# Optimization experiments

Hardware: AMD Instinct MI355X
Metric: run time of the kernel (lower is better)

Reference implementation:

```python
import jax, jax.numpy as jnp
import numpy as np

D_MODEL = 2048
N_HEADS = 16
D_HEAD = D_MODEL // N_HEADS  # 128


def setup_inputs() -> dict:
    key = jax.random.key(0)
    ks = jax.random.split(key, 5)
    b, t = 2, 2048
    s = 0.02
    return {
        "x": jax.random.normal(ks[0], (b, t, D_MODEL), dtype=jnp.float32),
        "Wq": jax.random.normal(ks[1], (D_MODEL, D_MODEL), dtype=jnp.float32) * s,
        "Wk": jax.random.normal(ks[2], (D_MODEL, D_HEAD), dtype=jnp.float32) * s,
        "Wv": jax.random.normal(ks[3], (D_MODEL, D_HEAD), dtype=jnp.float32) * s,
        "Wo": jax.random.normal(ks[4], (D_MODEL, D_MODEL), dtype=jnp.float32) * s,
    }


def reference(x, Wq, Wk, Wv, Wo):
    b, t, c = x.shape
    scale = D_HEAD ** -0.5
    # q: [b, h, t, d]; k, v: single shared KV head [b, s, d]
    q = (x @ Wq).reshape(b, t, N_HEADS, D_HEAD).transpose(0, 2, 1, 3)
    k = x @ Wk  # [b, s, d]
    v = x @ Wv  # [b, s, d]
    # broadcast the shared KV head across query heads without materializing copies
    scores = jnp.einsum('bhtd,bsd->bhts', q, k) * scale
    attn = jax.nn.softmax(scores, axis=-1)
    y = jnp.einsum('bhts,bsd->bhtd', attn, v)
    y = y.transpose(0, 2, 1, 3).reshape(b, t, c)
    return y @ Wo
```

## Files before the change

kernel.cpp:

```cpp
#include <hip/hip_runtime.h>

typedef unsigned short ushort_t;
typedef short bf16x8 __attribute__((ext_vector_type(8)));
typedef float f32x4 __attribute__((ext_vector_type(4)));

#define B_    2
#define T_    2048
#define C_    2048
#define H_    16
#define DH_   128
#define BT_   4096
#define NQKV  2304

#define OFF_XB   0UL
#define OFF_WT   16777216UL
#define OFF_WOT  26214400UL
#define OFF_QKV  34603008UL
#define OFF_VT   53477376UL
#define OFF_FLAG 54525952UL

__device__ __forceinline__ ushort_t f2bf(float f) {
  union { float f; unsigned u; } v; v.f = f;
  unsigned r = v.u + 0x7fffu + ((v.u >> 16) & 1u);
  return (ushort_t)(r >> 16);
}
__device__ __forceinline__ float bf2f(ushort_t u) {
  union { float f; unsigned u; } v; v.u = ((unsigned)u) << 16;
  return v.f;
}

__device__ __forceinline__ void gload_lds16(const ushort_t* g, ushort_t* l) {
  __builtin_amdgcn_global_load_lds((__attribute__((address_space(1))) void*)g,
                                   (__attribute__((address_space(3))) void*)l,
                                   16, 0, 0);
}

__global__ void detect_dtype(const ushort_t* x, int* flag) {
  if (threadIdx.x == 0 && blockIdx.x == 0) {
    int sane = 0;
    for (int i = 0; i < 32; ++i) {
      ushort_t u = x[2 * i];
      int e = (u >> 7) & 0xFF;
      if (u == 0 || (e >= 100 && e <= 140)) ++sane;
    }
    *flag = (sane >= 24) ? 1 : 0;
  }
}

__global__ __launch_bounds__(256) void cast_x(const void* __restrict__ xin,
                                              ushort_t* __restrict__ xb,
                                              const int* __restrict__ flag, int n8) {
  int i = blockIdx.x * 256 + threadIdx.x;
  if (i >= n8) return;
  if (*flag) {
    *(bf16x8*)(xb + (size_t)i * 8) = *(const bf16x8*)((const ushort_t*)xin + (size_t)i * 8);
  } else {
    const float* xf = (const float*)xin;
    f32x4 a = *(const f32x4*)(xf + (size_t)i * 8);
    f32x4 b = *(const f32x4*)(xf + (size_t)i * 8 + 4);
    bf16x8 o;
    o[0] = (short)f2bf(a[0]); o[1] = (short)f2bf(a[1]);
    o[2] = (short)f2bf(a[2]); o[3] = (short)f2bf(a[3]);
    o[4] = (short)f2bf(b[0]); o[5] = (short)f2bf(b[1]);
    o[6] = (short)f2bf(b[2]); o[7] = (short)f2bf(b[3]);
    *(bf16x8*)(xb + (size_t)i * 8) = o;
  }
}

__global__ __launch_bounds__(256) void transpose_cast(const void* __restrict__ src,
                                                      ushort_t* __restrict__ dst,
                                                      const int* __restrict__ flag,
                                                      int rows, int cols, int dst_ld,
                                                      int dst_row_off) {
  __shared__ float tile[32][33];
  int c0 = blockIdx.x * 32, r0 = blockIdx.y * 32;
  int tx = threadIdx.x & 31, ty = threadIdx.x >> 5;
  bool isbf = (*flag != 0);
#pragma unroll
  for (int j = 0; j < 4; ++j) {
    int r = r0 + ty + j * 8;
    float v;
    if (isbf) v = bf2f(((const ushort_t*)src)[(size_t)r * cols + c0 + tx]);
    else      v = ((const float*)src)[(size_t)r * cols + c0 + tx];
    tile[ty + j * 8][tx] = v;
  }
  __syncthreads();
#pragma unroll
  for (int j = 0; j < 4; ++j) {
    int c = c0 + ty + j * 8;
    dst[(size_t)(dst_row_off + c) * dst_ld + r0 + tx] = f2bf(tile[tx][ty + j * 8]);
  }
}

__global__ __launch_bounds__(256) void transpose_v(const ushort_t* __restrict__ qkv,
                                                   ushort_t* __restrict__ vT) {
  __shared__ ushort_t tile[32][33];
  int b = blockIdx.z;
  int t0 = blockIdx.x * 32, d0 = blockIdx.y * 32;
  int tx = threadIdx.x & 31, ty = threadIdx.x >> 5;
#pragma unroll
  for (int j = 0; j < 4; ++j) {
    int t = t0 + ty + j * 8;
    tile[ty + j * 8][tx] = qkv[(size_t)(b * T_ + t) * NQKV + 2176 + d0 + tx];
  }
  __syncthreads();
#pragma unroll
  for (int j = 0; j < 4; ++j) {
    int d = d0 + ty + j * 8;
    vT[(size_t)b * (DH_ * T_) + (size_t)d * T_ + t0 + tx] = tile[tx][ty + j * 8];
  }
}

__global__ __launch_bounds__(256) void gemm_bt(const ushort_t* __restrict__ A,
                                               const ushort_t* __restrict__ Bt,
                                               void* __restrict__ Cv,
                                               int M, int N, int K,
                                               int is_final, const int* __restrict__ flag) {
  __shared__ __align__(16) ushort_t As[128 * 32];
  __shared__ __align__(16) ushort_t Bs[128 * 32];
  const int tid = threadIdx.x;
  const int lane = tid & 63;
  const int wid = tid >> 6;
  const int m0 = blockIdx.y * 128;
  const int n0 = blockIdx.x * 128;
  const int wr = wid >> 1, wc = wid & 1;
  const int l15 = lane & 15, l4 = lane >> 4;

  f32x4 zero = {0.f, 0.f, 0.f, 0.f};
  f32x4 acc[4][4];
#pragma unroll
  for (int r = 0; r < 4; ++r)
#pragma unroll
    for (int c = 0; c < 4; ++c) acc[r][c] = zero;

  const ushort_t* ga = A + (size_t)(m0 + (tid >> 2)) * K + (tid & 3) * 8;
  const ushort_t* gb = Bt + (size_t)(n0 + (tid >> 2)) * K + (tid & 3) * 8;
  ushort_t* lA = As + wid * 512;
  ushort_t* lB = Bs + wid * 512;
  const size_t stride64 = (size_t)64 * K;

  for (int k0 = 0; k0 < K; k0 += 32) {
    __syncthreads();
    gload_lds16(ga + k0, lA);
    gload_lds16(ga + k0 + stride64, lA + 2048);
    gload_lds16(gb + k0, lB);
    gload_lds16(gb + k0 + stride64, lB + 2048);
    __syncthreads();

    bf16x8 af[4], bfr[4];
#pragma unroll
    for (int r = 0; r < 4; ++r)
      af[r] = *(const bf16x8*)&As[(wr * 64 + r * 16 + l15) * 32 + l4 * 8];
#pragma unroll
    for (int c = 0; c < 4; ++c)
      bfr[c] = *(const bf16x8*)&Bs[(wc * 64 + c * 16 + l15) * 32 + l4 * 8];
#pragma unroll
    for (int r = 0; r < 4; ++r)
#pragma unroll
      for (int c = 0; c < 4; ++c)
        acc[r][c] = __builtin_amdgcn_mfma_f32_16x16x32_bf16(af[r], bfr[c], acc[r][c], 0, 0, 0);
  }

  const bool f32out = is_final && (*flag == 0);
#pragma unroll
  for (int r = 0; r < 4; ++r) {
#pragma unroll
    for (int c = 0; c < 4; ++c) {
      int row = m0 + wr * 64 + r * 16 + l4 * 4;
      int col = n0 + wc * 64 + c * 16 + l15;
#pragma unroll
      for (int g = 0; g < 4; ++g) {
        if (f32out) ((float*)Cv)[(size_t)(row + g) * N + col] = acc[r][c][g];
        else ((ushort_t*)Cv)[(size_t)(row + g) * N + col] = f2bf(acc[r][c][g]);
      }
    }
  }
}

__global__ __launch_bounds__(512, 4) void attn_kernel(const ushort_t* __restrict__ qkv,
                                                      const ushort_t* __restrict__ vT,
                                                      ushort_t* __restrict__ y) {
  __shared__ __align__(16) ushort_t Ks[64 * 128];
  __shared__ __align__(16) ushort_t Vs[128 * 64];
  __shared__ __align__(16) ushort_t Pl[8][16][72];

  const int tid = threadIdx.x;
  const int lane = tid & 63;
  const int wid = tid >> 6;
  const int h = blockIdx.y * 2 + (wid >> 2);
  const int b = blockIdx.z;
  const int tb = b * T_;
  const int q0 = blockIdx.x * 64 + (wid & 3) * 16;
  const int l15 = lane & 15, l4 = lane >> 4;

  bf16x8 qf[4];
  {
    const ushort_t* qbase = qkv + (size_t)(tb + q0 + l15) * NQKV + h * DH_ + l4 * 8;
#pragma unroll
    for (int ks = 0; ks < 4; ++ks) qf[ks] = *(const bf16x8*)(qbase + ks * 32);
  }

  const ushort_t* ksrc[2];
  const ushort_t* vsrc[2];
  ushort_t* kdst[2];
  ushort_t* vdst[2];
#pragma unroll
  for (int it = 0; it < 2; ++it) {
    int id = tid + it * 512;
    int krow = id >> 4, kslot = id & 15;
    ksrc[it] = qkv + (size_t)(tb + krow) * NQKV + 2048 + ((kslot ^ (krow & 7)) << 3);
    kdst[it] = Ks + (size_t)(it * 512 + (wid << 6)) * 8;
    int vrow = id >> 3, vslot = id & 7;
    vsrc[it] = vT + (size_t)b * (DH_ * T_) + (size_t)vrow * T_ + ((vslot ^ (vrow & 7)) << 3);
    vdst[it] = Vs + (size_t)(it * 512 + (wid << 6)) * 8;
  }

  f32x4 zero = {0.f, 0.f, 0.f, 0.f};
  f32x4 o[8];
#pragma unroll
  for (int i = 0; i < 8; ++i) o[i] = zero;
  float mrow[4] = {-1e30f, -1e30f, -1e30f, -1e30f};
  float lrow[4] = {0.f, 0.f, 0.f, 0.f};
  const float sc = 0.08838834764831845f;

  for (int st = 0; st < 32; ++st) {
    const int s0 = st * 64;
    __syncthreads();
    gload_lds16(ksrc[0] + (size_t)s0 * NQKV, kdst[0]);
    gload_lds16(ksrc[1] + (size_t)s0 * NQKV, kdst[1]);
    gload_lds16(vsrc[0] + s0, vdst[0]);
    gload_lds16(vsrc[1] + s0, vdst[1]);
    __syncthreads();

    f32x4 sa[4];
#pragma unroll
    for (int c = 0; c < 4; ++c) {
      sa[c] = zero;
      int srow = c * 16 + l15;
      int sw = srow & 7;
#pragma unroll
      for (int ks = 0; ks < 4; ++ks) {
        bf16x8 kf = *(const bf16x8*)&Ks[srow * 128 + (((ks * 4 + l4) ^ sw) << 3)];
        sa[c] = __builtin_amdgcn_mfma_f32_16x16x32_bf16(qf[ks], kf, sa[c], 0, 0, 0);
      }
    }

    float alpha[4];
#pragma unroll
    for (int r = 0; r < 4; ++r) {
#pragma unroll
      for (int c = 0; c < 4; ++c) sa[c][r] *= sc;
      float m = fmaxf(fmaxf(sa[0][r], sa[1][r]), fmaxf(sa[2][r], sa[3][r]));
      m = fmaxf(m, __shfl_xor(m, 1));
      m = fmaxf(m, __shfl_xor(m, 2));
      m = fmaxf(m, __shfl_xor(m, 4));
      m = fmaxf(m, __shfl_xor(m, 8));
      float mn = fmaxf(mrow[r], m);
      alpha[r] = __expf(mrow[r] - mn);
      mrow[r] = mn;
      float s = 0.f;
#pragma unroll
      for (int c = 0; c < 4; ++c) {
        float p = __expf(sa[c][r] - mn);
        sa[c][r] = p;
        s += p;
      }
      s += __shfl_xor(s, 1);
      s += __shfl_xor(s, 2);
      s += __shfl_xor(s, 4);
      s += __shfl_xor(s, 8);
      lrow[r] = lrow[r] * alpha[r] + s;
    }

#pragma unroll
    for (int c = 0; c < 4; ++c)
#pragma unroll
      for (int r = 0; r < 4; ++r)
        Pl[wid][l4 * 4 + r][c * 16 + l15] = f2bf(sa[c][r]);

#pragma unroll
    for (int nb = 0; nb < 8; ++nb)
#pragma unroll
      for (int r = 0; r < 4; ++r) o[nb][r] *= alpha[r];

    bf16x8 pa0 = *(const bf16x8*)&Pl[wid][l15][l4 * 8];
    bf16x8 pa1 = *(const bf16x8*)&Pl[wid][l15][32 + l4 * 8];
#pragma unroll
    for (int nb = 0; nb < 8; ++nb) {
      int vrow = nb * 16 + l15;
      int sw = vrow & 7;
      bf16x8 vb0 = *(const bf16x8*)&Vs[vrow * 64 + ((l4 ^ sw) << 3)];
      o[nb] = __builtin_amdgcn_mfma_f32_16x16x32_bf16(pa0, vb0, o[nb], 0, 0, 0);
      bf16x8 vb1 = *(const bf16x8*)&Vs[vrow * 64 + (((4 + l4) ^ sw) << 3)];
      o[nb] = __builtin_amdgcn_mfma_f32_16x16x32_bf16(pa1, vb1, o[nb], 0, 0, 0);
    }
  }

#pragma unroll
  for (int nb = 0; nb < 8; ++nb) {
#pragma unroll
    for (int r = 0; r < 4; ++r) {
      int qrow = tb + q0 + l4 * 4 + r;
      y[(size_t)qrow * C_ + h * DH_ + nb * 16 + l15] = f2bf(o[nb][r] / lrow[r]);
    }
  }
}

extern "C" void kernel_launch(void* const* d_in, const int* in_sizes, int n_in,
                              void* d_out, int out_size, void* d_ws, size_t ws_size,
                              hipStream_t stream) {
  (void)in_sizes; (void)n_in; (void)out_size; (void)ws_size;
  const void* x  = d_in[0];
  const void* Wq = d_in[1];
  const void* Wk = d_in[2];
  const void* Wv = d_in[3];
  const void* Wo = d_in[4];

  char* ws = (char*)d_ws;
  ushort_t* xb  = (ushort_t*)(ws + OFF_XB);
  ushort_t* WT  = (ushort_t*)(ws + OFF_WT);
  ushort_t* WoT = (ushort_t*)(ws + OFF_WOT);
  ushort_t* qkv = (ushort_t*)(ws + OFF_QKV);
  ushort_t* vTp = (ushort_t*)(ws + OFF_VT);
  int* flag     = (int*)(ws + OFF_FLAG);

  detect_dtype<<<1, 1, 0, stream>>>((const ushort_t*)x, flag);

  cast_x<<<4096, 256, 0, stream>>>(x, xb, flag, (BT_ * C_) / 8);

  transpose_cast<<<dim3(64, 64), 256, 0, stream>>>(Wq, WT, flag, 2048, 2048, 2048, 0);
  transpose_cast<<<dim3(4, 64), 256, 0, stream>>>(Wk, WT, flag, 2048, 128, 2048, 2048);
  transpose_cast<<<dim3(4, 64), 256, 0, stream>>>(Wv, WT, flag, 2048, 128, 2048, 2176);
  transpose_cast<<<dim3(64, 64), 256, 0, stream>>>(Wo, WoT, flag, 2048, 2048, 2048, 0);

  gemm_bt<<<dim3(NQKV / 128, BT_ / 128), 256, 0, stream>>>(xb, WT, qkv, BT_, NQKV, C_, 0, flag);

  transpose_v<<<dim3(T_ / 32, DH_ / 32, B_), 256, 0, stream>>>(qkv, vTp);

  attn_kernel<<<dim3(T_ / 64, H_ / 2, B_), 512, 0, stream>>>(qkv, vTp, xb);

  gemm_bt<<<dim3(C_ / 128, BT_ / 128), 256, 0, stream>>>(xb, WoT, d_out, BT_, C_, C_, 1, flag);
}
```

Before: 395.9 us.

## Double-buffer attention K/V tiles, fold softmax scale into Q, lazy rescale

The attention kernel now double-buffers K and V tiles in LDS, issuing the next tile's global-to-LDS loads before computing on the current one, so one of the two barriers per step goes away. The softmax scale and log2(e) are folded into the Q projection's GEMM epilogue so the kernel can use exp2 directly. The score MFMA operands are swapped (transposed layout) so each lane owns one query row, which makes the max and sum reductions cheaper. The P matrix is packed with v_cvt_pk_bf16 and redistributed through register shuffles instead of an LDS round-trip. Online-softmax rescaling is skipped when the running max grows by 8 or less (log2 units), which saves work but lets exponents grow up to 2^8 before renormalizing.

```diff
diff --git a/kernel.cpp b/kernel.cpp
--- a/kernel.cpp
+++ b/kernel.cpp
@@ -27,6 +27,16 @@
 __device__ __forceinline__ float bf2f(ushort_t u) {
   union { float f; unsigned u; } v; v.u = ((unsigned)u) << 16;
   return v.f;
+}
+__device__ __forceinline__ int cvtpk_bf16(float lo, float hi) {
+  int r;
+  asm("v_cvt_pk_bf16_f32 %0, %1, %2" : "=v"(r) : "v"(lo), "v"(hi));
+  return r;
+}
+__device__ __forceinline__ bf16x8 mkfrag(int d0, int d1, int d2, int d3) {
+  union { int i[4]; bf16x8 v; } u;
+  u.i[0] = d0; u.i[1] = d1; u.i[2] = d2; u.i[3] = d3;
+  return u.v;
 }
 
 __device__ __forceinline__ void gload_lds16(const ushort_t* g, ushort_t* l) {
@@ -115,7 +125,8 @@
                                                const ushort_t* __restrict__ Bt,
                                                void* __restrict__ Cv,
                                                int M, int N, int K,
-                                               int is_final, const int* __restrict__ flag) {
+                                               int is_final, const int* __restrict__ flag,
+                                               float qscale, int qcols) {
   __shared__ __align__(16) ushort_t As[128 * 32];
   __shared__ __align__(16) ushort_t Bs[128 * 32];
   const int tid = threadIdx.x;
@@ -168,10 +179,12 @@
     for (int c = 0; c < 4; ++c) {
       int row = m0 + wr * 64 + r * 16 + l4 * 4;
       int col = n0 + wc * 64 + c * 16 + l15;
+      float s = (col < qcols) ? qscale : 1.0f;
 #pragma unroll
       for (int g = 0; g < 4; ++g) {
-        if (f32out) ((float*)Cv)[(size_t)(row + g) * N + col] = acc[r][c][g];
-        else ((ushort_t*)Cv)[(size_t)(row + g) * N + col] = f2bf(acc[r][c][g]);
+        float v = acc[r][c][g] * s;
+        if (f32out) ((float*)Cv)[(size_t)(row + g) * N + col] = v;
+        else ((ushort_t*)Cv)[(size_t)(row + g) * N + col] = f2bf(v);
       }
     }
   }
@@ -180,9 +193,8 @@
 __global__ __launch_bounds__(512, 4) void attn_kernel(const ushort_t* __restrict__ qkv,
                                                       const ushort_t* __restrict__ vT,
                                                       ushort_t* __restrict__ y) {
-  __shared__ __align__(16) ushort_t Ks[64 * 128];
-  __shared__ __align__(16) ushort_t Vs[128 * 64];
-  __shared__ __align__(16) ushort_t Pl[8][16][72];
+  __shared__ __align__(16) ushort_t Ks[2][64 * 128];
+  __shared__ __align__(16) ushort_t Vs[2][128 * 64];
 
   const int tid = threadIdx.x;
   const int lane = tid & 63;
@@ -200,37 +212,44 @@
     for (int ks = 0; ks < 4; ++ks) qf[ks] = *(const bf16x8*)(qbase + ks * 32);
   }
 
-  const ushort_t* ksrc[2];
-  const ushort_t* vsrc[2];
-  ushort_t* kdst[2];
-  ushort_t* vdst[2];
+  const ushort_t* ksrcb[2];
+  const ushort_t* vsrcb[2];
+  int koff[2], voff[2];
 #pragma unroll
   for (int it = 0; it < 2; ++it) {
     int id = tid + it * 512;
     int krow = id >> 4, kslot = id & 15;
-    ksrc[it] = qkv + (size_t)(tb + krow) * NQKV + 2048 + ((kslot ^ (krow & 7)) << 3);
-    kdst[it] = Ks + (size_t)(it * 512 + (wid << 6)) * 8;
+    ksrcb[it] = qkv + (size_t)(tb + krow) * NQKV + 2048 + ((kslot ^ (krow & 7)) << 3);
     int vrow = id >> 3, vslot = id & 7;
-    vsrc[it] = vT + (size_t)b * (DH_ * T_) + (size_t)vrow * T_ + ((vslot ^ (vrow & 7)) << 3);
-    vdst[it] = Vs + (size_t)(it * 512 + (wid << 6)) * 8;
+    vsrcb[it] = vT + (size_t)b * (DH_ * T_) + (size_t)vrow * T_ + ((vslot ^ (vrow & 7)) << 3);
+    koff[it] = (it * 512 + (wid << 6)) * 8;
+    voff[it] = (it * 512 + (wid << 6)) * 8;
   }
 
   f32x4 zero = {0.f, 0.f, 0.f, 0.f};
   f32x4 o[8];
 #pragma unroll
   for (int i = 0; i < 8; ++i) o[i] = zero;
-  float mrow[4] = {-1e30f, -1e30f, -1e30f, -1e30f};
-  float lrow[4] = {0.f, 0.f, 0.f, 0.f};
-  const float sc = 0.08838834764831845f;
+  float m_s = -1e30f;
+  float l_s = 0.f;
+
+#pragma unroll
+  for (int it = 0; it < 2; ++it) {
+    gload_lds16(ksrcb[it], &Ks[0][koff[it]]);
+    gload_lds16(vsrcb[it], &Vs[0][voff[it]]);
+  }
 
   for (int st = 0; st < 32; ++st) {
-    const int s0 = st * 64;
+    const int cur = st & 1;
     __syncthreads();
-    gload_lds16(ksrc[0] + (size_t)s0 * NQKV, kdst[0]);
-    gload_lds16(ksrc[1] + (size_t)s0 * NQKV, kdst[1]);
-    gload_lds16(vsrc[0] + s0, vdst[0]);
-    gload_lds16(vsrc[1] + s0, vdst[1]);
-    __syncthreads();
+    if (st < 31) {
+      const int s1 = (st + 1) * 64;
+#pragma unroll
+      for (int it = 0; it < 2; ++it) {
+        gload_lds16(ksrcb[it] + (size_t)s1 * NQKV, &Ks[cur ^ 1][koff[it]]);
+        gload_lds16(vsrcb[it] + s1, &Vs[cur ^ 1][voff[it]]);
+      }
+    }
 
     f32x4 sa[4];
 #pragma unroll
@@ -240,68 +259,90 @@
       int sw = srow & 7;
 #pragma unroll
       for (int ks = 0; ks < 4; ++ks) {
-        bf16x8 kf = *(const bf16x8*)&Ks[srow * 128 + (((ks * 4 + l4) ^ sw) << 3)];
-        sa[c] = __builtin_amdgcn_mfma_f32_16x16x32_bf16(qf[ks], kf, sa[c], 0, 0, 0);
+        bf16x8 kf = *(const bf16x8*)&Ks[cur][srow * 128 + (((ks * 4 + l4) ^ sw) << 3)];
+        sa[c] = __builtin_amdgcn_mfma_f32_16x16x32_bf16(kf, qf[ks], sa[c], 0, 0, 0);
       }
     }
 
-    float alpha[4];
-#pragma unroll
-    for (int r = 0; r < 4; ++r) {
-#pragma unroll
-      for (int c = 0; c < 4; ++c) sa[c][r] *= sc;
-      float m = fmaxf(fmaxf(sa[0][r], sa[1][r]), fmaxf(sa[2][r], sa[3][r]));
-      m = fmaxf(m, __shfl_xor(m, 1));
-      m = fmaxf(m, __shfl_xor(m, 2));
-      m = fmaxf(m, __shfl_xor(m, 4));
-      m = fmaxf(m, __shfl_xor(m, 8));
-      float mn = fmaxf(mrow[r], m);
-      alpha[r] = __expf(mrow[r] - mn);
-      mrow[r] = mn;
-      float s = 0.f;
-#pragma unroll
-      for (int c = 0; c < 4; ++c) {
-        float p = __expf(sa[c][r] - mn);
+    float pmax = sa[0][0];
+#pragma unroll
+    for (int c = 0; c < 4; ++c)
+#pragma unroll
+      for (int r = 0; r < 4; ++r) pmax = fmaxf(pmax, sa[c][r]);
+    pmax = fmaxf(pmax, __shfl_xor(pmax, 16));
+    pmax = fmaxf(pmax, __shfl_xor(pmax, 32));
+
+    if (!__all(pmax - m_s <= 8.0f)) {
+      float mn = fmaxf(m_s, pmax);
+      float al = exp2f(m_s - mn);
+      m_s = mn;
+      l_s *= al;
+      float ar[4];
+#pragma unroll
+      for (int r = 0; r < 4; ++r) ar[r] = __shfl(al, l4 * 4 + r);
+#pragma unroll
+      for (int nb = 0; nb < 8; ++nb)
+#pragma unroll
+        for (int r = 0; r < 4; ++r) o[nb][r] *= ar[r];
+    }
+
+    float ps = 0.f;
+#pragma unroll
+    for (int c = 0; c < 4; ++c)
+#pragma unroll
+      for (int r = 0; r < 4; ++r) {
+        float p = exp2f(sa[c][r] - m_s);
         sa[c][r] = p;
-        s += p;
+        ps += p;
       }
-      s += __shfl_xor(s, 1);
-      s += __shfl_xor(s, 2);
-      s += __shfl_xor(s, 4);
-      s += __shfl_xor(s, 8);
-      lrow[r] = lrow[r] * alpha[r] + s;
-    }
-
-#pragma unroll
-    for (int c = 0; c < 4; ++c)
-#pragma unroll
-      for (int r = 0; r < 4; ++r)
-        Pl[wid][l4 * 4 + r][c * 16 + l15] = f2bf(sa[c][r]);
-
-#pragma unroll
-    for (int nb = 0; nb < 8; ++nb)
-#pragma unroll
-      for (int r = 0; r < 4; ++r) o[nb][r] *= alpha[r];
-
-    bf16x8 pa0 = *(const bf16x8*)&Pl[wid][l15][l4 * 8];
-    bf16x8 pa1 = *(const bf16x8*)&Pl[wid][l15][32 + l4 * 8];
+    ps += __shfl_xor(ps, 16);
+    ps += __shfl_xor(ps, 32);
+    l_s += ps;
+
+    int pk0[2], pk1[2], pk2[2], pk3[2];
+    pk0[0] = cvtpk_bf16(sa[0][0], sa[0][1]); pk0[1] = cvtpk_bf16(sa[0][2], sa[0][3]);
+    pk1[0] = cvtpk_bf16(sa[1][0], sa[1][1]); pk1[1] = cvtpk_bf16(sa[1][2], sa[1][3]);
+    pk2[0] = cvtpk_bf16(sa[2][0], sa[2][1]); pk2[1] = cvtpk_bf16(sa[2][2], sa[2][3]);
+    pk3[0] = cvtpk_bf16(sa[3][0], sa[3][1]); pk3[1] = cvtpk_bf16(sa[3][2], sa[3][3]);
+
+    const int srcA = ((lane >> 4) & 1) * 32 + l15;
+    const int srcB = srcA + 16;
+    const bool cHi = lane >= 32;
+
+    int a00 = __shfl(pk0[0], srcA), a01 = __shfl(pk0[1], srcA);
+    int a02 = __shfl(pk0[0], srcB), a03 = __shfl(pk0[1], srcB);
+    int b00 = __shfl(pk1[0], srcA), b01 = __shfl(pk1[1], srcA);
+    int b02 = __shfl(pk1[0], srcB), b03 = __shfl(pk1[1], srcB);
+    bf16x8 pa0 = mkfrag(cHi ? b00 : a00, cHi ? b01 : a01,
+                        cHi ? b02 : a02, cHi ? b03 : a03);
+
+    int a10 = __shfl(pk2[0], srcA), a11 = __shfl(pk2[1], srcA);
+    int a12 = __shfl(pk2[0], srcB), a13 = __shfl(pk2[1], srcB);
+    int b10 = __shfl(pk3[0], srcA), b11 = __shfl(pk3[1], srcA);
+    int b12 = __shfl(pk3[0], srcB), b13 = __shfl(pk3[1], srcB);
+    bf16x8 pa1 = mkfrag(cHi ? b10 : a10, cHi ? b11 : a11,
+                        cHi ? b12 : a12, cHi ? b13 : a13);
+
 #pragma unroll
     for (int nb = 0; nb < 8; ++nb) {
       int vrow = nb * 16 + l15;
       int sw = vrow & 7;
-      bf16x8 vb0 = *(const bf16x8*)&Vs[vrow * 64 + ((l4 ^ sw) << 3)];
+      bf16x8 vb0 = *(const bf16x8*)&Vs[cur][vrow * 64 + ((l4 ^ sw) << 3)];
       o[nb] = __builtin_amdgcn_mfma_f32_16x16x32_bf16(pa0, vb0, o[nb], 0, 0, 0);
-      bf16x8 vb1 = *(const bf16x8*)&Vs[vrow * 64 + (((4 + l4) ^ sw) << 3)];
+      bf16x8 vb1 = *(const bf16x8*)&Vs[cur][vrow * 64 + (((4 + l4) ^ sw) << 3)];
       o[nb] = __builtin_amdgcn_mfma_f32_16x16x32_bf16(pa1, vb1, o[nb], 0, 0, 0);
     }
   }
 
+  float lr[4];
+#pragma unroll
+  for (int r = 0; r < 4; ++r) lr[r] = __shfl(l_s, l4 * 4 + r);
 #pragma unroll
   for (int nb = 0; nb < 8; ++nb) {
 #pragma unroll
     for (int r = 0; r < 4; ++r) {
       int qrow = tb + q0 + l4 * 4 + r;
-      y[(size_t)qrow * C_ + h * DH_ + nb * 16 + l15] = f2bf(o[nb][r] / lrow[r]);
+      y[(size_t)qrow * C_ + h * DH_ + nb * 16 + l15] = f2bf(o[nb][r] / lr[r]);
     }
   }
 }
@@ -333,11 +374,12 @@
   transpose_cast<<<dim3(4, 64), 256, 0, stream>>>(Wv, WT, flag, 2048, 128, 2048, 2176);
   transpose_cast<<<dim3(64, 64), 256, 0, stream>>>(Wo, WoT, flag, 2048, 2048, 2048, 0);
 
-  gemm_bt<<<dim3(NQKV / 128, BT_ / 128), 256, 0, stream>>>(xb, WT, qkv, BT_, NQKV, C_, 0, flag);
+  const float k1 = 0.08838834764831845f * 1.4426950408889634f;
+  gemm_bt<<<dim3(NQKV / 128, BT_ / 128), 256, 0, stream>>>(xb, WT, qkv, BT_, NQKV, C_, 0, flag, k1, 2048);
 
   transpose_v<<<dim3(T_ / 32, DH_ / 32, B_), 256, 0, stream>>>(qkv, vTp);
 
   attn_kernel<<<dim3(T_ / 64, H_ / 2, B_), 512, 0, stream>>>(qkv, vTp, xb);
 
-  gemm_bt<<<dim3(C_ / 128, BT_ / 128), 256, 0, stream>>>(xb, WoT, d_out, BT_, C_, C_, 1, flag);
-}
+  gemm_bt<<<dim3(C_ / 128, BT_ / 128), 256, 0, stream>>>(xb, WoT, d_out, BT_, C_, C_, 1, flag, 1.0f, 0);
+}
```

Result: faster. 363.2 us (-8.2%).
